# Optimization experiments

Hardware: AMD Instinct MI355X
Metric: run time of the kernel (lower is better)

The kernel has to match this reference:

```python
import jax, jax.numpy as jnp
import numpy as np

D_MODEL = 192; D_INNER = 384; D_STATE = 16; DT_RANK = 12; D_CONV = 4; DEPTH = 24
IMG = 256; PATCH = 16; BATCH = 32; NPATCH = (IMG // PATCH) ** 2; SEQ = NPATCH + 1; EPS = 1e-5


def setup_inputs() -> dict:
    key = jax.random.key(0)
    ks = iter(jax.random.split(key, 64))
    def rn(shape, s=0.02):
        return jax.random.normal(next(ks), shape, jnp.float32) * s
    inp = {}
    inp['x'] = jax.random.normal(next(ks), (BATCH, 3, IMG, IMG), jnp.float32)
    inp['patch_w'] = rn((D_MODEL, 3, PATCH, PATCH), 0.02)
    inp['patch_b'] = jnp.zeros((D_MODEL,), jnp.float32)
    inp['cls_token'] = rn((1, 1, D_MODEL), 0.02)
    inp['pos_embed'] = rn((1, SEQ, D_MODEL), 0.02)
    inp['norm_w'] = jnp.ones((DEPTH, D_MODEL), jnp.float32)
    inp['in_proj_w'] = rn((DEPTH, 2 * D_INNER, D_MODEL), 0.05)
    A_init = jnp.log(jnp.arange(1, D_STATE + 1, dtype=jnp.float32))  # S4D-real init
    for sfx in ['', '_b']:
        inp['conv_w' + sfx] = rn((DEPTH, D_INNER, D_CONV), 0.2)
        inp['conv_b' + sfx] = jnp.zeros((DEPTH, D_INNER), jnp.float32)
        inp['xproj_w' + sfx] = rn((DEPTH, DT_RANK + 2 * D_STATE, D_INNER), 0.05)
        inp['dtproj_w' + sfx] = rn((DEPTH, D_INNER, DT_RANK), 0.1)
        inp['dt_bias' + sfx] = rn((DEPTH, D_INNER), 0.5) - 4.0  # softplus(~-4) ~ small dt
        inp['A_log' + sfx] = jnp.broadcast_to(A_init, (DEPTH, D_INNER, D_STATE)).copy()
        inp['Dskip' + sfx] = jnp.ones((DEPTH, D_INNER), jnp.float32)
    inp['out_proj_w'] = rn((DEPTH, D_MODEL, D_INNER), 0.05)
    inp['norm_f_w'] = jnp.ones((D_MODEL,), jnp.float32)
    return inp


def _silu(v):
    return v * jax.nn.sigmoid(v)


def _rmsnorm(v, w):
    v = v.astype(jnp.float32)
    return v * jax.lax.rsqrt(jnp.mean(v * v, axis=-1, keepdims=True) + EPS) * w


def _ssm_branch(xin, z, conv_w, conv_b, xproj_w, dt_w, dt_b, A_log, Dp):
    # xin, z: (B, L, Di). One direction of the Mamba selective scan.
    B, L, Di = xin.shape
    pad = D_CONV - 1
    xp = jnp.pad(xin, ((0, 0), (pad, 0), (0, 0)))  # causal depthwise conv
    xc = sum(xp[:, k:k + L, :] * conv_w[:, k] for k in range(D_CONV)) + conv_b
    xc = _silu(xc)
    proj = jnp.einsum('bld,pd->blp', xc, xproj_w)  # (B,L,dt_rank+2N)
    dt_lo, Bm, Cm = jnp.split(proj, [DT_RANK, DT_RANK + D_STATE], axis=-1)
    dt = jax.nn.softplus(jnp.einsum('blr,dr->bld', dt_lo, dt_w) + dt_b)  # (B,L,Di)
    A = -jnp.exp(A_log)  # (Di, N)

    def step(h, inps):
        dt_t, B_t, C_t, x_t = inps  # (B,Di),(B,N),(B,N),(B,Di)
        dA = jnp.exp(dt_t[..., None] * A)                       # (B,Di,N)
        h = h * dA + (dt_t * x_t)[..., None] * B_t[:, None, :]  # ZOH discretization
        y = jnp.einsum('bdn,bn->bd', h, C_t)
        return h, y

    tm = lambda a: jnp.swapaxes(a, 0, 1)  # time-major
    h0 = jnp.zeros((B, Di, D_STATE), xin.dtype)
    _, ys = jax.lax.scan(step, h0, (tm(dt), tm(Bm), tm(Cm), tm(xc)))
    y = tm(ys) + Dp * xc
    return y * _silu(z)


def reference(x, patch_w, patch_b, cls_token, pos_embed, norm_w, in_proj_w,
              conv_w, conv_b, xproj_w, dtproj_w, dt_bias, A_log, Dskip,
              conv_w_b, conv_b_b, xproj_w_b, dtproj_w_b, dt_bias_b, A_log_b, Dskip_b,
              out_proj_w, norm_f_w):
    B = x.shape[0]
    # Patch embedding: Conv2d(3, D, k=16, s=16) -> (B, M, D)
    feat = jax.lax.conv_general_dilated(x, patch_w, (PATCH, PATCH), 'VALID',
                                        dimension_numbers=('NCHW', 'OIHW', 'NCHW'))
    feat = feat + patch_b[None, :, None, None]
    feat = feat.reshape(B, D_MODEL, NPATCH).transpose(0, 2, 1)
    # middle cls token insertion
    pos = NPATCH // 2
    cls = jnp.broadcast_to(cls_token, (B, 1, D_MODEL))
    h = jnp.concatenate([feat[:, :pos], cls, feat[:, pos:]], axis=1) + pos_embed
    residual = None
    flip = lambda a: a[:, ::-1]
    for i in range(DEPTH):
        # fused add + RMSNorm (prenorm), residual in fp32
        residual = h.astype(jnp.float32) if residual is None else (residual + h.astype(jnp.float32))
        hn = _rmsnorm(residual, norm_w[i])
        # Mamba mixer, bimamba v2 (shared in/out proj, separate scan params)
        xz = jnp.einsum('bld,ed->ble', hn, in_proj_w[i])
        xin, z = jnp.split(xz, 2, axis=-1)
        y_f = _ssm_branch(xin, z, conv_w[i], conv_b[i], xproj_w[i], dtproj_w[i],
                          dt_bias[i], A_log[i], Dskip[i])
        y_r = flip(_ssm_branch(flip(xin), flip(z), conv_w_b[i], conv_b_b[i], xproj_w_b[i],
                               dtproj_w_b[i], dt_bias_b[i], A_log_b[i], Dskip_b[i]))
        y = (y_f + y_r) * 0.5  # if_divide_out=True
        h = jnp.einsum('bld,od->blo', y, out_proj_w[i])
    # final fused add + RMSNorm (prenorm=False)
    out = _rmsnorm(residual + h.astype(jnp.float32), norm_f_w)
    return out
```

## Files before the change

### kernel.cpp

```cpp
#include <hip/hip_runtime.h>
#include <hip/hip_bf16.h>
#include <math.h>

#define D_MODEL 192
#define D_INNER 384
#define D_STATE 16
#define DT_RANK 12
#define DEPTH   24
#define SEQL    257
#define BATCH   32
#define NTOK    (BATCH*SEQL)
#define NC      16
#define CL      17
#define CCH     32

typedef unsigned short ushort_t;
using bf16x8 = __attribute__((ext_vector_type(8))) short;
using f32x4  = __attribute__((ext_vector_type(4))) float;

__device__ __forceinline__ ushort_t f2b(float f) {
    __hip_bfloat16 h = __float2bfloat16(f);
    return reinterpret_cast<ushort_t&>(h);
}
__device__ __forceinline__ float b2f(ushort_t u) {
    __hip_bfloat16 h;
    reinterpret_cast<ushort_t&>(h) = u;
    return __bfloat162float(h);
}
__device__ __forceinline__ float softplus_f(float v) {
    return (v > 20.f) ? v : log1pf(expf(v));
}
__device__ __forceinline__ float softplus_fast(float v) {
    float e = __expf(v);
    float lg = __logf(1.f + e);
    return (v > 20.f) ? v : lg;
}

__device__ __forceinline__ void pow_ladder(float r1, float* dA) {
    float r2 = r1 * r1;
    float r3 = r2 * r1;
    float r4 = r2 * r2;
    float r8 = r4 * r4;
    float r12 = r8 * r4;
    dA[0] = r1;       dA[1] = r2;       dA[2] = r3;       dA[3] = r4;
    dA[4] = r4 * r1;  dA[5] = r4 * r2;  dA[6] = r4 * r3;  dA[7] = r8;
    dA[8] = r8 * r1;  dA[9] = r8 * r2;  dA[10] = r8 * r3; dA[11] = r12;
    dA[12] = r12 * r1; dA[13] = r12 * r2; dA[14] = r12 * r3; dA[15] = r8 * r8;
}

__global__ __launch_bounds__(256) void convert_k(const float* __restrict__ in, ushort_t* __restrict__ out, int n) {
    int i = (blockIdx.x * 256 + threadIdx.x) * 4;
    if (i + 3 < n) {
        float4 v = *(const float4*)(in + i);
        ushort4 o;
        o.x = f2b(v.x); o.y = f2b(v.y); o.z = f2b(v.z); o.w = f2b(v.w);
        *(ushort4*)(out + i) = o;
    } else {
        for (int j = i; j < n; j++) out[j] = f2b(in[j]);
    }
}

__global__ __launch_bounds__(256) void checkA_k(const float* __restrict__ Al, const float* __restrict__ Alb,
                                                int* __restrict__ flag) {
    int i = blockIdx.x * 256 + threadIdx.x;
    const int total = DEPTH * 384 * 16;
    if (i >= total) return;
    int n = i & 15;
    float tgt = (float)(n + 1);
    float a = __expf(Al[i]);
    float b = __expf(Alb[i]);
    if (fabsf(a - tgt) > 1e-4f * tgt || fabsf(b - tgt) > 1e-4f * tgt) atomicAnd(flag, 0);
}

__global__ __launch_bounds__(256) void rearrange_k(const float* __restrict__ x, ushort_t* __restrict__ Ap) {
    size_t i = (size_t)blockIdx.x * 256 + threadIdx.x;
    const size_t total = (size_t)8192 * 768 / 4;
    if (i >= total) return;
    size_t o = i * 4;
    int bt  = (int)(o / 768);
    int rem = (int)(o % 768);
    int c  = rem >> 8;
    int r2 = rem & 255;
    int pi = r2 >> 4;
    int pj = r2 & 15;
    int b = bt >> 8;
    int t = bt & 255;
    int ph = t >> 4, pw = t & 15;
    size_t src = (((size_t)(b * 3 + c) * 256) + (size_t)(ph * 16 + pi)) * 256 + (pw * 16 + pj);
    float4 v = *(const float4*)(x + src);
    ushort4 ov;
    ov.x = f2b(v.x); ov.y = f2b(v.y); ov.z = f2b(v.z); ov.w = f2b(v.w);
    *(ushort4*)(Ap + o) = ov;
}

__global__ __launch_bounds__(192) void assemble_k(const float* __restrict__ P, const float* __restrict__ pb,
                                                  const float* __restrict__ cls, const float* __restrict__ pos,
                                                  float* __restrict__ hb) {
    int o = threadIdx.x;
    int l = blockIdx.x;
    int b = blockIdx.y;
    float v;
    if (l == 128) {
        v = cls[o];
    } else {
        int t = (l < 128) ? l : l - 1;
        v = P[((size_t)b * 256 + t) * 192 + o] + pb[o];
    }
    hb[((size_t)b * SEQL + l) * 192 + o] = v + pos[l * 192 + o];
}

template<int FINAL>
__global__ __launch_bounds__(192) void addnorm_k(float* res, const float* __restrict__ h,
                                                 const float* __restrict__ w, void* __restrict__ outp) {
    int row = blockIdx.x;
    int t = threadIdx.x;
    size_t idx = (size_t)row * 192 + t;
    float r = res[idx] + h[idx];
    if (!FINAL) res[idx] = r;
    float ss = r * r;
    #pragma unroll
    for (int o = 32; o > 0; o >>= 1) ss += __shfl_down(ss, o);
    __shared__ float ps[3];
    int wid = t >> 6;
    if ((t & 63) == 0) ps[wid] = ss;
    __syncthreads();
    float tot = ps[0] + ps[1] + ps[2];
    float inv = rsqrtf(tot / 192.f + 1e-5f);
    float v = r * inv * w[t];
    if (FINAL) ((float*)outp)[idx] = v;
    else       ((ushort_t*)outp)[idx] = f2b(v);
}

template<int OUTBF>
__global__ __launch_bounds__(256) void gemm_bf16(const ushort_t* __restrict__ A,
                                                 const ushort_t* __restrict__ W,
                                                 void* __restrict__ C,
                                                 int M, int N, int K, int ldc) {
    __shared__ ushort_t As[128 * 40];
    __shared__ ushort_t Bs[64 * 40];
    int tid = threadIdx.x;
    int m0 = blockIdx.y * 128, n0 = blockIdx.x * 64;
    int row = tid >> 2;
    int k8  = (tid & 3) * 8;
    int lane = tid & 63;
    int w = tid >> 6;
    int wr = w >> 1, wc = w & 1;
    int lr = lane & 15;
    int lk = (lane >> 4) * 8;
    f32x4 acc[4][2];
    #pragma unroll
    for (int i = 0; i < 4; i++)
        #pragma unroll
        for (int j = 0; j < 2; j++) acc[i][j] = (f32x4){0.f, 0.f, 0.f, 0.f};

    for (int k0 = 0; k0 < K; k0 += 32) {
        #pragma unroll
        for (int hhalf = 0; hhalf < 2; hhalf++) {
            int r = row + hhalf * 64;
            int m = m0 + r;
            bf16x8 v = {0,0,0,0,0,0,0,0};
            if (m < M) v = *(const bf16x8*)(A + (size_t)m * K + k0 + k8);
            *(bf16x8*)(&As[r * 40 + k8]) = v;
        }
        {
            int n = n0 + row;
            bf16x8 v = {0,0,0,0,0,0,0,0};
            if (n < N) v = *(const bf16x8*)(W + (size_t)n * K + k0 + k8);
            *(bf16x8*)(&Bs[row * 40 + k8]) = v;
        }
        __syncthreads();
        bf16x8 af[4], bfr[2];
        #pragma unroll
        for (int mi = 0; mi < 4; mi++)
            af[mi] = *(const bf16x8*)(&As[(wr * 64 + mi * 16 + lr) * 40 + lk]);
        #pragma unroll
        for (int ni = 0; ni < 2; ni++)
            bfr[ni] = *(const bf16x8*)(&Bs[(wc * 32 + ni * 16 + lr) * 40 + lk]);
        #pragma unroll
        for (int mi = 0; mi < 4; mi++)
            #pragma unroll
            for (int ni = 0; ni < 2; ni++)
                acc[mi][ni] = __builtin_amdgcn_mfma_f32_16x16x32_bf16(af[mi], bfr[ni], acc[mi][ni], 0, 0, 0);
        __syncthreads();
    }
    int rbase = (lane >> 4) * 4;
    #pragma unroll
    for (int mi = 0; mi < 4; mi++) {
        #pragma unroll
        for (int ni = 0; ni < 2; ni++) {
            #pragma unroll
            for (int r = 0; r < 4; r++) {
                int m = m0 + wr * 64 + mi * 16 + rbase + r;
                int n = n0 + wc * 32 + ni * 16 + lr;
                if (m < M && n < N) {
                    if (OUTBF) ((ushort_t*)C)[(size_t)m * ldc + n] = f2b(acc[mi][ni][r]);
                    else       ((float*)C)[(size_t)m * ldc + n] = acc[mi][ni][r];
                }
            }
        }
    }
}

__global__ __launch_bounds__(256) void gemm_xproj(const ushort_t* __restrict__ A0, const ushort_t* __restrict__ A1,
                                                  const ushort_t* __restrict__ W0, const ushort_t* __restrict__ W1,
                                                  float* __restrict__ C0, float* __restrict__ C1,
                                                  int M, int N, int K, int ldc) {
    __shared__ ushort_t As[64 * 40];
    __shared__ ushort_t Bs[64 * 40];
    int dir = blockIdx.z;
    const ushort_t* A = dir ? A1 : A0;
    const ushort_t* W = dir ? W1 : W0;
    float* C = dir ? C1 : C0;
    int tid = threadIdx.x;
    int m0 = blockIdx.y * 64, n0 = blockIdx.x * 64;
    int row = tid >> 2;
    int k8  = (tid & 3) * 8;
    int lane = tid & 63;
    int w = tid >> 6;
    int wr = w >> 1, wc = w & 1;
    int lr = lane & 15;
    int lk = (lane >> 4) * 8;
    f32x4 acc[2][2];
    #pragma unroll
    for (int i = 0; i < 2; i++)
        #pragma unroll
        for (int j = 0; j < 2; j++) acc[i][j] = (f32x4){0.f, 0.f, 0.f, 0.f};

    for (int k0 = 0; k0 < K; k0 += 32) {
        {
            int m = m0 + row;
            bf16x8 v = {0,0,0,0,0,0,0,0};
            if (m < M) v = *(const bf16x8*)(A + (size_t)m * K + k0 + k8);
            *(bf16x8*)(&As[row * 40 + k8]) = v;
            int n = n0 + row;
            bf16x8 wv = {0,0,0,0,0,0,0,0};
            if (n < N) wv = *(const bf16x8*)(W + (size_t)n * K + k0 + k8);
            *(bf16x8*)(&Bs[row * 40 + k8]) = wv;
        }
        __syncthreads();
        bf16x8 af[2], bfr[2];
        #pragma unroll
        for (int mi = 0; mi < 2; mi++)
            af[mi] = *(const bf16x8*)(&As[(wr * 32 + mi * 16 + lr) * 40 + lk]);
        #pragma unroll
        for (int ni = 0; ni < 2; ni++)
            bfr[ni] = *(const bf16x8*)(&Bs[(wc * 32 + ni * 16 + lr) * 40 + lk]);
        #pragma unroll
        for (int mi = 0; mi < 2; mi++)
            #pragma unroll
            for (int ni = 0; ni < 2; ni++)
                acc[mi][ni] = __builtin_amdgcn_mfma_f32_16x16x32_bf16(af[mi], bfr[ni], acc[mi][ni], 0, 0, 0);
        __syncthreads();
    }
    int rbase = (lane >> 4) * 4;
    #pragma unroll
    for (int mi = 0; mi < 2; mi++) {
        #pragma unroll
        for (int ni = 0; ni < 2; ni++) {
            #pragma unroll
            for (int r = 0; r < 4; r++) {
                int m = m0 + wr * 32 + mi * 16 + rbase + r;
                int n = n0 + wc * 32 + ni * 16 + lr;
                if (m < M && n < N) C[(size_t)m * ldc + n] = acc[mi][ni][r];
            }
        }
    }
}

__global__ __launch_bounds__(256) void gemm_out(const ushort_t* __restrict__ yf, const ushort_t* __restrict__ yr,
                                                const ushort_t* __restrict__ W, float* __restrict__ C,
                                                int M, int N, int K, int ldc) {
    __shared__ ushort_t As[64 * 40];
    __shared__ ushort_t Bs[64 * 40];
    int tid = threadIdx.x;
    int m0 = blockIdx.y * 64, n0 = blockIdx.x * 64;
    int row = tid >> 2;
    int k8  = (tid & 3) * 8;
    int lane = tid & 63;
    int w = tid >> 6;
    int wr = w >> 1, wc = w & 1;
    int lr = lane & 15;
    int lk = (lane >> 4) * 8;
    int m_ld = m0 + row;
    int mok = (m_ld < M);
    int bb = m_ld / SEQL;
    int ll = m_ld - bb * SEQL;
    size_t rowf = (size_t)m_ld * 384;
    size_t rowr = ((size_t)bb * SEQL + (SEQL - 1 - ll)) * 384;
    f32x4 acc[2][2];
    #pragma unroll
    for (int i = 0; i < 2; i++)
        #pragma unroll
        for (int j = 0; j < 2; j++) acc[i][j] = (f32x4){0.f, 0.f, 0.f, 0.f};

    for (int k0 = 0; k0 < K; k0 += 32) {
        {
            bf16x8 v = {0,0,0,0,0,0,0,0};
            if (mok) {
                bf16x8 vf = *(const bf16x8*)(yf + rowf + k0 + k8);
                bf16x8 vr = *(const bf16x8*)(yr + rowr + k0 + k8);
                #pragma unroll
                for (int j = 0; j < 8; j++) {
                    float a = b2f((ushort_t)vf[j]);
                    float b2 = b2f((ushort_t)vr[j]);
                    v[j] = (short)f2b(0.5f * (a + b2));
                }
            }
            *(bf16x8*)(&As[row * 40 + k8]) = v;
            int n = n0 + row;
            bf16x8 wv = {0,0,0,0,0,0,0,0};
            if (n < N) wv = *(const bf16x8*)(W + (size_t)n * K + k0 + k8);
            *(bf16x8*)(&Bs[row * 40 + k8]) = wv;
        }
        __syncthreads();
        bf16x8 af[2], bfr[2];
        #pragma unroll
        for (int mi = 0; mi < 2; mi++)
            af[mi] = *(const bf16x8*)(&As[(wr * 32 + mi * 16 + lr) * 40 + lk]);
        #pragma unroll
        for (int ni = 0; ni < 2; ni++)
            bfr[ni] = *(const bf16x8*)(&Bs[(wc * 32 + ni * 16 + lr) * 40 + lk]);
        #pragma unroll
        for (int mi = 0; mi < 2; mi++)
            #pragma unroll
            for (int ni = 0; ni < 2; ni++)
                acc[mi][ni] = __builtin_amdgcn_mfma_f32_16x16x32_bf16(af[mi], bfr[ni], acc[mi][ni], 0, 0, 0);
        __syncthreads();
    }
    int rbase = (lane >> 4) * 4;
    #pragma unroll
    for (int mi = 0; mi < 2; mi++) {
        #pragma unroll
        for (int ni = 0; ni < 2; ni++) {
            #pragma unroll
            for (int r = 0; r < 4; r++) {
                int m = m0 + wr * 32 + mi * 16 + rbase + r;
                int n = n0 + wc * 32 + ni * 16 + lr;
                if (m < M && n < N) C[(size_t)m * ldc + n] = acc[mi][ni][r];
            }
        }
    }
}

__global__ __launch_bounds__(384) void conv_silu_k(const ushort_t* __restrict__ xz,
                                                   const float* __restrict__ cw, const float* __restrict__ cb,
                                                   const float* __restrict__ cwb, const float* __restrict__ cbb,
                                                   ushort_t* __restrict__ xcf, ushort_t* __restrict__ xcr) {
    int d = threadIdx.x;
    int lc = blockIdx.x;
    int b = blockIdx.y;
    int dir = blockIdx.z;
    int lstart = lc * CCH;
    int lend = (lstart + CCH < SEQL) ? (lstart + CCH) : SEQL;
    const float* w = dir ? cwb : cw;
    const float* bias = dir ? cbb : cb;
    float4 wv = *(const float4*)(w + d * 4);
    float bs = bias[d];
    ushort_t* out = dir ? xcr : xcf;
    size_t base = (size_t)b * SEQL;
    float win0 = 0.f, win1 = 0.f, win2 = 0.f;
    if (lstart - 3 >= 0) win0 = b2f(xz[(base + (dir ? (SEQL-1-(lstart-3)) : (lstart-3))) * 768 + d]);
    if (lstart - 2 >= 0) win1 = b2f(xz[(base + (dir ? (SEQL-1-(lstart-2)) : (lstart-2))) * 768 + d]);
    if (lstart - 1 >= 0) win2 = b2f(xz[(base + (dir ? (SEQL-1-(lstart-1)) : (lstart-1))) * 768 + d]);
    float xcur = b2f(xz[(base + (dir ? (SEQL-1-lstart) : lstart)) * 768 + d]);
    for (int l = lstart; l < lend; l++) {
        int ln = l + 1;
        float xnext = 0.f;
        if (ln < lend) xnext = b2f(xz[(base + (dir ? (SEQL-1-ln) : ln)) * 768 + d]);
        float a = bs;
        a = fmaf(wv.x, win0, a);
        a = fmaf(wv.y, win1, a);
        a = fmaf(wv.z, win2, a);
        a = fmaf(wv.w, xcur, a);
        float s = a / (1.f + __expf(-a));
        out[(base + l) * 384 + d] = f2b(s);
        win0 = win1; win1 = win2; win2 = xcur; xcur = xnext;
    }
}

__global__ __launch_bounds__(192) void scan_p1(const ushort_t* __restrict__ xcf, const ushort_t* __restrict__ xcr,
                                               const float* __restrict__ dtbcf, const float* __restrict__ dtbcr,
                                               const float* __restrict__ dwf, const float* __restrict__ dwr,
                                               const float* __restrict__ dbf, const float* __restrict__ dbr,
                                               const float* __restrict__ Alf, const float* __restrict__ Alb,
                                               float* __restrict__ Sbuf, float* __restrict__ sumdt,
                                               const int* __restrict__ flagp) {
    int t = threadIdx.x;
    int d0 = t, d1 = t + 192;
    int c = blockIdx.x;
    int b = blockIdx.y, dir = blockIdx.z;
    int bd = b * 2 + dir;
    const ushort_t* xcp = dir ? xcr : xcf;
    const float* pbc = (dir ? dtbcr : dtbcf) + (size_t)b * SEQL * 44;
    int lstart = c * CL;
    int clen = (lstart + CL < SEQL) ? CL : (SEQL - lstart);
    size_t rowbase = (size_t)b * SEQL + lstart;

    float dw0[12], dw1[12];
    {
        const float* dwp = (dir ? dwr : dwf);
        #pragma unroll
        for (int r = 0; r < 12; r++) dw0[r] = dwp[d0 * 12 + r];
        #pragma unroll
        for (int r = 0; r < 12; r++) dw1[r] = dwp[d1 * 12 + r];
    }
    float db0 = (dir ? dbr : dbf)[d0];
    float db1 = (dir ? dbr : dbf)[d1];
    bool fast = (*flagp != 0);
    float S0[16], S1[16];
    #pragma unroll
    for (int n = 0; n < 16; n++) { S0[n] = 0.f; S1[n] = 0.f; }
    float ss0 = 0.f, ss1 = 0.f;

    if (fast) {
        float x0 = b2f(xcp[rowbase * 384 + d0]);
        float x1 = b2f(xcp[rowbase * 384 + d1]);
        for (int l = 0; l < clen; l++) {
            int ln = (l + 1 < clen) ? (l + 1) : l;
            float x0n = b2f(xcp[(rowbase + ln) * 384 + d0]);
            float x1n = b2f(xcp[(rowbase + ln) * 384 + d1]);
            const float* rp = pbc + (size_t)(lstart + l) * 44;
            float4 t0 = *(const float4*)(rp);
            float4 t1 = *(const float4*)(rp + 4);
            float4 t2 = *(const float4*)(rp + 8);
            float4 B0 = *(const float4*)(rp + 12);
            float4 B1 = *(const float4*)(rp + 16);
            float4 B2 = *(const float4*)(rp + 20);
            float4 B3 = *(const float4*)(rp + 24);
            float tv[12] = {t0.x,t0.y,t0.z,t0.w, t1.x,t1.y,t1.z,t1.w, t2.x,t2.y,t2.z,t2.w};
            float a0 = db0, a1 = db1;
            #pragma unroll
            for (int r = 0; r < 12; r++) {
                a0 = fmaf(tv[r], dw0[r], a0);
                a1 = fmaf(tv[r], dw1[r], a1);
            }
            float dt0 = softplus_fast(a0);
            float dt1 = softplus_fast(a1);
            ss0 += dt0; ss1 += dt1;
            float dtx0 = dt0 * x0, dtx1 = dt1 * x1;
            float dA0[16], dA1[16];
            pow_ladder(__expf(-dt0), dA0);
            pow_ladder(__expf(-dt1), dA1);
            float Bv[16] = {B0.x,B0.y,B0.z,B0.w, B1.x,B1.y,B1.z,B1.w,
                            B2.x,B2.y,B2.z,B2.w, B3.x,B3.y,B3.z,B3.w};
            #pragma unroll
            for (int n = 0; n < 16; n++) {
                S0[n] = fmaf(S0[n], dA0[n], dtx0 * Bv[n]);
                S1[n] = fmaf(S1[n], dA1[n], dtx1 * Bv[n]);
            }
            x0 = x0n; x1 = x1n;
        }
    } else {
        const float* alog = (dir ? Alb : Alf);
        float A0[16], A1[16];
        #pragma unroll
        for (int n = 0; n < 16; n++) A0[n] = -__expf(alog[d0 * 16 + n]);
        #pragma unroll
        for (int n = 0; n < 16; n++) A1[n] = -__expf(alog[d1 * 16 + n]);
        for (int l = 0; l < clen; l++) {
            const float* rp = pbc + (size_t)(lstart + l) * 44;
            float a0 = db0, a1 = db1;
            #pragma unroll
            for (int r = 0; r < 12; r++) {
                a0 = fmaf(rp[r], dw0[r], a0);
                a1 = fmaf(rp[r], dw1[r], a1);
            }
            float dt0 = softplus_f(a0);
            float dt1 = softplus_f(a1);
            ss0 += dt0; ss1 += dt1;
            float x0 = b2f(xcp[(rowbase + l) * 384 + d0]);
            float x1 = b2f(xcp[(rowbase + l) * 384 + d1]);
            float dtx0 = dt0 * x0, dtx1 = dt1 * x1;
            #pragma unroll
            for (int n = 0; n < 16; n++) {
                S0[n] = fmaf(S0[n], __expf(dt0 * A0[n]), dtx0 * rp[12 + n]);
                S1[n] = fmaf(S1[n], __expf(dt1 * A1[n]), dtx1 * rp[12 + n]);
            }
        }
    }
    float* spb = Sbuf + ((size_t)bd * NC + c) * 6144;
    #pragma unroll
    for (int j = 0; j < 4; j++) {
        *(float4*)(spb + d0 * 16 + j * 4) = make_float4(S0[j*4], S0[j*4+1], S0[j*4+2], S0[j*4+3]);
        *(float4*)(spb + d1 * 16 + j * 4) = make_float4(S1[j*4], S1[j*4+1], S1[j*4+2], S1[j*4+3]);
    }
    sumdt[((size_t)bd * NC + c) * 384 + d0] = ss0;
    sumdt[((size_t)bd * NC + c) * 384 + d1] = ss1;
}

__global__ __launch_bounds__(256) void scan_mid(float* __restrict__ Sbuf, const float* __restrict__ sumdt,
                                                const float* __restrict__ Alf, const float* __restrict__ Alb,
                                                const int* __restrict__ flagp) {
    int gid = blockIdx.x * 256 + threadIdx.x;
    int n = gid & 15;
    int rest = gid >> 4;
    int d = rest % 384;
    int bd = rest / 384;
    int dir = bd & 1;
    bool fast = (*flagp != 0);
    float A = fast ? -(float)(n + 1) : -__expf((dir ? Alb : Alf)[d * 16 + n]);
    float h = 0.f;
    #pragma unroll
    for (int c = 0; c < NC; c++) {
        size_t si = ((size_t)bd * NC + c) * 6144 + d * 16 + n;
        float S = Sbuf[si];
        float sd = sumdt[((size_t)bd * NC + c) * 384 + d];
        Sbuf[si] = h;
        h = fmaf(h, __expf(A * sd), S);
    }
}

__global__ __launch_bounds__(192) void scan_p3(const ushort_t* __restrict__ xcf, const ushort_t* __restrict__ xcr,
                                               const float* __restrict__ dtbcf, const float* __restrict__ dtbcr,
                                               const float* __restrict__ dwf, const float* __restrict__ dwr,
                                               const float* __restrict__ dbf, const float* __restrict__ dbr,
                                               const float* __restrict__ Alf, const float* __restrict__ Alb,
                                               const float* __restrict__ Df, const float* __restrict__ Db,
                                               const ushort_t* __restrict__ xz,
                                               const float* __restrict__ Sbuf,
                                               ushort_t* __restrict__ ybf, ushort_t* __restrict__ ybr,
                                               const int* __restrict__ flagp) {
    int t = threadIdx.x;
    int d0 = t, d1 = t + 192;
    int c = blockIdx.x;
    int b = blockIdx.y, dir = blockIdx.z;
    int bd = b * 2 + dir;
    const ushort_t* xcp = dir ? xcr : xcf;
    const float* pbc = (dir ? dtbcr : dtbcf) + (size_t)b * SEQL * 44;
    ushort_t* yb = dir ? ybr : ybf;
    int lstart = c * CL;
    int clen = (lstart + CL < SEQL) ? CL : (SEQL - lstart);
    size_t rowbase = (size_t)b * SEQL + lstart;
    size_t seqbase = (size_t)b * SEQL;

    float dw0[12], dw1[12];
    {
        const float* dwp = (dir ? dwr : dwf);
        #pragma unroll
        for (int r = 0; r < 12; r++) dw0[r] = dwp[d0 * 12 + r];
        #pragma unroll
        for (int r = 0; r < 12; r++) dw1[r] = dwp[d1 * 12 + r];
    }
    float db0 = (dir ? dbr : dbf)[d0];
    float db1 = (dir ? dbr : dbf)[d1];
    float Dp0 = (dir ? Db : Df)[d0];
    float Dp1 = (dir ? Db : Df)[d1];
    bool fast = (*flagp != 0);
    float h0[16], h1[16];
    {
        const float* spb = Sbuf + ((size_t)bd * NC + c) * 6144;
        #pragma unroll
        for (int j = 0; j < 4; j++) {
            float4 hv0 = *(const float4*)(spb + d0 * 16 + j * 4);
            float4 hv1 = *(const float4*)(spb + d1 * 16 + j * 4);
            h0[j*4] = hv0.x; h0[j*4+1] = hv0.y; h0[j*4+2] = hv0.z; h0[j*4+3] = hv0.w;
            h1[j*4] = hv1.x; h1[j*4+1] = hv1.y; h1[j*4+2] = hv1.z; h1[j*4+3] = hv1.w;
        }
    }

    if (fast) {
        float x0 = b2f(xcp[rowbase * 384 + d0]);
        float x1 = b2f(xcp[rowbase * 384 + d1]);
        size_t zr0 = (dir ? (seqbase + SEQL - 1 - lstart) : rowbase) * 768 + 384;
        float z0 = b2f(xz[zr0 + d0]);
        float z1 = b2f(xz[zr0 + d1]);
        for (int l = 0; l < clen; l++) {
            int ln = (l + 1 < clen) ? (l + 1) : l;
            float x0n = b2f(xcp[(rowbase + ln) * 384 + d0]);
            float x1n = b2f(xcp[(rowbase + ln) * 384 + d1]);
            size_t zrn = (dir ? (seqbase + SEQL - 1 - (lstart + ln)) : (rowbase + ln)) * 768 + 384;
            float z0n = b2f(xz[zrn + d0]);
            float z1n = b2f(xz[zrn + d1]);
            const float* rp = pbc + (size_t)(lstart + l) * 44;
            float4 t0 = *(const float4*)(rp);
            float4 t1 = *(const float4*)(rp + 4);
            float4 t2 = *(const float4*)(rp + 8);
            float4 B0 = *(const float4*)(rp + 12);
            float4 B1 = *(const float4*)(rp + 16);
            float4 B2 = *(const float4*)(rp + 20);
            float4 B3 = *(const float4*)(rp + 24);
            float4 C0 = *(const float4*)(rp + 28);
            float4 C1 = *(const float4*)(rp + 32);
            float4 C2 = *(const float4*)(rp + 36);
            float4 C3 = *(const float4*)(rp + 40);
            float tv[12] = {t0.x,t0.y,t0.z,t0.w, t1.x,t1.y,t1.z,t1.w, t2.x,t2.y,t2.z,t2.w};
            float a0 = db0, a1 = db1;
            #pragma unroll
            for (int r = 0; r < 12; r++) {
                a0 = fmaf(tv[r], dw0[r], a0);
                a1 = fmaf(tv[r], dw1[r], a1);
            }
            float dt0 = softplus_fast(a0);
            float dt1 = softplus_fast(a1);
            float dtx0 = dt0 * x0, dtx1 = dt1 * x1;
            float dA0[16], dA1[16];
            pow_ladder(__expf(-dt0), dA0);
            pow_ladder(__expf(-dt1), dA1);
            float Bv[16] = {B0.x,B0.y,B0.z,B0.w, B1.x,B1.y,B1.z,B1.w,
                            B2.x,B2.y,B2.z,B2.w, B3.x,B3.y,B3.z,B3.w};
            float Cv[16] = {C0.x,C0.y,C0.z,C0.w, C1.x,C1.y,C1.z,C1.w,
                            C2.x,C2.y,C2.z,C2.w, C3.x,C3.y,C3.z,C3.w};
            float y0 = 0.f, y1 = 0.f;
            #pragma unroll
            for (int n = 0; n < 16; n++) {
                h0[n] = fmaf(h0[n], dA0[n], dtx0 * Bv[n]);
                h1[n] = fmaf(h1[n], dA1[n], dtx1 * Bv[n]);
                y0 = fmaf(h0[n], Cv[n], y0);
                y1 = fmaf(h1[n], Cv[n], y1);
            }
            y0 = fmaf(Dp0, x0, y0);
            y1 = fmaf(Dp1, x1, y1);
            float sz0 = z0 / (1.f + __expf(-z0));
            float sz1 = z1 / (1.f + __expf(-z1));
            yb[(rowbase + l) * 384 + d0] = f2b(y0 * sz0);
            yb[(rowbase + l) * 384 + d1] = f2b(y1 * sz1);
            x0 = x0n; x1 = x1n; z0 = z0n; z1 = z1n;
        }
    } else {
        const float* alog = (dir ? Alb : Alf);
        float A0[16], A1[16];
        #pragma unroll
        for (int n = 0; n < 16; n++) A0[n] = -__expf(alog[d0 * 16 + n]);
        #pragma unroll
        for (int n = 0; n < 16; n++) A1[n] = -__expf(alog[d1 * 16 + n]);
        for (int l = 0; l < clen; l++) {
            const float* rp = pbc + (size_t)(lstart + l) * 44;
            float a0 = db0, a1 = db1;
            #pragma unroll
            for (int r = 0; r < 12; r++) {
                a0 = fmaf(rp[r], dw0[r], a0);
                a1 = fmaf(rp[r], dw1[r], a1);
            }
            float dt0 = softplus_f(a0);
            float dt1 = softplus_f(a1);
            float x0 = b2f(xcp[(rowbase + l) * 384 + d0]);
            float x1 = b2f(xcp[(rowbase + l) * 384 + d1]);
            size_t zr = (dir ? (seqbase + SEQL - 1 - (lstart + l)) : (rowbase + l)) * 768 + 384;
            float z0 = b2f(xz[zr + d0]);
            float z1 = b2f(xz[zr + d1]);
            float dtx0 = dt0 * x0, dtx1 = dt1 * x1;
            float y0 = 0.f, y1 = 0.f;
            #pragma unroll
            for (int n = 0; n < 16; n++) {
                h0[n] = fmaf(h0[n], __expf(dt0 * A0[n]), dtx0 * rp[12 + n]);
                h1[n] = fmaf(h1[n], __expf(dt1 * A1[n]), dtx1 * rp[12 + n]);
                y0 = fmaf(h0[n], rp[28 + n], y0);
                y1 = fmaf(h1[n], rp[28 + n], y1);
            }
            y0 = fmaf(Dp0, x0, y0);
            y1 = fmaf(Dp1, x1, y1);
            float sz0 = z0 / (1.f + __expf(-z0));
            float sz1 = z1 / (1.f + __expf(-z1));
            yb[(rowbase + l) * 384 + d0] = f2b(y0 * sz0);
            yb[(rowbase + l) * 384 + d1] = f2b(y1 * sz1);
        }
    }
}

extern "C" void kernel_launch(void* const* d_in, const int* in_sizes, int n_in,
                              void* d_out, int out_size, void* d_ws, size_t ws_size,
                              hipStream_t stream) {
    const float* x         = (const float*)d_in[0];
    const float* patch_w   = (const float*)d_in[1];
    const float* patch_b   = (const float*)d_in[2];
    const float* cls_token = (const float*)d_in[3];
    const float* pos_embed = (const float*)d_in[4];
    const float* norm_w    = (const float*)d_in[5];
    const float* in_proj_w = (const float*)d_in[6];
    const float* conv_w    = (const float*)d_in[7];
    const float* conv_b    = (const float*)d_in[8];
    const float* xproj_w   = (const float*)d_in[9];
    const float* dtproj_w  = (const float*)d_in[10];
    const float* dt_bias   = (const float*)d_in[11];
    const float* A_log     = (const float*)d_in[12];
    const float* Dskip     = (const float*)d_in[13];
    const float* conv_w_b  = (const float*)d_in[14];
    const float* conv_b_b  = (const float*)d_in[15];
    const float* xproj_w_b = (const float*)d_in[16];
    const float* dtproj_w_b= (const float*)d_in[17];
    const float* dt_bias_b = (const float*)d_in[18];
    const float* A_log_b   = (const float*)d_in[19];
    const float* Dskip_b   = (const float*)d_in[20];
    const float* out_proj_w= (const float*)d_in[21];
    const float* norm_f_w  = (const float*)d_in[22];

    float* ws = (float*)d_ws;
    size_t off = 0;
    float* res   = ws + off; off += (size_t)NTOK * 192;
    float* hbuf  = ws + off; off += (size_t)NTOK * 192;
    ushort_t* xzb = (ushort_t*)(ws + off); off += (size_t)NTOK * 384;
    ushort_t* hnb = (ushort_t*)(ws + off); off += (size_t)NTOK * 96;
    ushort_t* xcfb = (ushort_t*)(ws + off); off += (size_t)NTOK * 192;
    ushort_t* xcrb = (ushort_t*)(ws + off); off += (size_t)NTOK * 192;
    float* dtbcf = ws + off; off += (size_t)NTOK * 44;
    float* dtbcr = ws + off; off += (size_t)NTOK * 44;
    ushort_t* ybf = (ushort_t*)(ws + off); off += (size_t)NTOK * 192;
    ushort_t* ybr = (ushort_t*)(ws + off); off += (size_t)NTOK * 192;
    float* Sbuf  = ws + off; off += (size_t)BATCH * 2 * NC * 6144;
    float* sumdt = ws + off; off += (size_t)BATCH * 2 * NC * 384;
    int* flagp   = (int*)(ws + off); off += 4;
    ushort_t* wb = (ushort_t*)(ws + off);
    ushort_t* winb   = wb;
    ushort_t* woutb  = winb  + 3538944;
    ushort_t* xpfb   = woutb + 1769472;
    ushort_t* xprb   = xpfb  + 405504;
    ushort_t* patchwb= xprb  + 405504;

    ushort_t* Apatch = xzb;
    float* Ppatch = Sbuf;

    convert_k<<<(3538944/4 + 255)/256, 256, 0, stream>>>(in_proj_w, winb, 3538944);
    convert_k<<<(1769472/4 + 255)/256, 256, 0, stream>>>(out_proj_w, woutb, 1769472);
    convert_k<<<(405504/4 + 255)/256, 256, 0, stream>>>(xproj_w, xpfb, 405504);
    convert_k<<<(405504/4 + 255)/256, 256, 0, stream>>>(xproj_w_b, xprb, 405504);
    convert_k<<<(147456/4 + 255)/256, 256, 0, stream>>>(patch_w, patchwb, 147456);

    hipMemsetAsync(res, 0, (size_t)NTOK * 192 * sizeof(float), stream);
    hipMemsetAsync(flagp, 1, 4, stream);
    checkA_k<<<(DEPTH*384*16 + 255)/256, 256, 0, stream>>>(A_log, A_log_b, flagp);

    rearrange_k<<<6144, 256, 0, stream>>>(x, Apatch);
    gemm_bf16<0><<<dim3(3, 64), 256, 0, stream>>>(Apatch, patchwb, Ppatch, 8192, 192, 768, 192);
    assemble_k<<<dim3(SEQL, BATCH), 192, 0, stream>>>(Ppatch, patch_b, cls_token, pos_embed, hbuf);

    for (int i = 0; i < DEPTH; i++) {
        const float* nw   = norm_w + i * 192;
        const float* cwf  = conv_w + (size_t)i * 384 * 4;
        const float* cbf  = conv_b + (size_t)i * 384;
        const float* cwr  = conv_w_b + (size_t)i * 384 * 4;
        const float* cbr  = conv_b_b + (size_t)i * 384;
        const float* dpf  = dtproj_w + (size_t)i * 384 * 12;
        const float* dpr  = dtproj_w_b + (size_t)i * 384 * 12;
        const float* dbf  = dt_bias + (size_t)i * 384;
        const float* dbr  = dt_bias_b + (size_t)i * 384;
        const float* alf  = A_log + (size_t)i * 384 * 16;
        const float* alr  = A_log_b + (size_t)i * 384 * 16;
        const float* dsf  = Dskip + (size_t)i * 384;
        const float* dsr  = Dskip_b + (size_t)i * 384;

        addnorm_k<0><<<NTOK, 192, 0, stream>>>(res, hbuf, nw, hnb);
        gemm_bf16<1><<<dim3(12, 65), 256, 0, stream>>>(hnb, winb + (size_t)i * 768 * 192, xzb,
                                                       NTOK, 768, 192, 768);
        conv_silu_k<<<dim3((SEQL + CCH - 1) / CCH, BATCH, 2), 384, 0, stream>>>(xzb, cwf, cbf, cwr, cbr, xcfb, xcrb);
        gemm_xproj<<<dim3(1, 129, 2), 256, 0, stream>>>(xcfb, xcrb,
                                                        xpfb + (size_t)i * 44 * 384, xprb + (size_t)i * 44 * 384,
                                                        dtbcf, dtbcr, NTOK, 44, 384, 44);
        scan_p1<<<dim3(NC, BATCH, 2), 192, 0, stream>>>(xcfb, xcrb, dtbcf, dtbcr,
                                                        dpf, dpr, dbf, dbr, alf, alr, Sbuf, sumdt, flagp);
        scan_mid<<<(BATCH * 2 * 384 * 16) / 256, 256, 0, stream>>>(Sbuf, sumdt, alf, alr, flagp);
        scan_p3<<<dim3(NC, BATCH, 2), 192, 0, stream>>>(xcfb, xcrb, dtbcf, dtbcr,
                                                        dpf, dpr, dbf, dbr, alf, alr, dsf, dsr,
                                                        xzb, Sbuf, ybf, ybr, flagp);
        gemm_out<<<dim3(3, 129), 256, 0, stream>>>(ybf, ybr, woutb + (size_t)i * 192 * 384, hbuf,
                                                   NTOK, 192, 384, 192);
    }

    addnorm_k<1><<<NTOK, 192, 0, stream>>>(res, hbuf, norm_f_w, (float*)d_out);
}
```

Measured before the change: 3.051 ms.

## Fuse out-projection GEMM with residual add and next-layer RMSNorm

Replaces the separate out_proj GEMM and the following add+RMSNorm kernel with one kernel whose blocks each cover 32 full rows of all 192 output columns. The residual add and row norm are done in the GEMM epilogue through shuffle and shared-memory reductions. This removes one launch per layer and the round trip of the fp32 hbuf through memory. In exchange the GEMM tile shape changes to 32x192, and only half the threads load A, which may lower load efficiency. NTOK/32 divides evenly, so no bounds checks are needed.

```diff
diff --git a/kernel.cpp b/kernel.cpp
--- a/kernel.cpp
+++ b/kernel.cpp
@@ -109,14 +109,13 @@
     hb[((size_t)b * SEQL + l) * 192 + o] = v + pos[l * 192 + o];
 }
 
-template<int FINAL>
 __global__ __launch_bounds__(192) void addnorm_k(float* res, const float* __restrict__ h,
-                                                 const float* __restrict__ w, void* __restrict__ outp) {
+                                                 const float* __restrict__ w, ushort_t* __restrict__ outp) {
     int row = blockIdx.x;
     int t = threadIdx.x;
     size_t idx = (size_t)row * 192 + t;
     float r = res[idx] + h[idx];
-    if (!FINAL) res[idx] = r;
+    res[idx] = r;
     float ss = r * r;
     #pragma unroll
     for (int o = 32; o > 0; o >>= 1) ss += __shfl_down(ss, o);
@@ -126,9 +125,7 @@
     __syncthreads();
     float tot = ps[0] + ps[1] + ps[2];
     float inv = rsqrtf(tot / 192.f + 1e-5f);
-    float v = r * inv * w[t];
-    if (FINAL) ((float*)outp)[idx] = v;
-    else       ((ushort_t*)outp)[idx] = f2b(v);
+    outp[idx] = f2b(r * inv * w[t]);
 }
 
 template<int OUTBF>
@@ -267,76 +264,132 @@
     }
 }
 
-__global__ __launch_bounds__(256) void gemm_out(const ushort_t* __restrict__ yf, const ushort_t* __restrict__ yr,
-                                                const ushort_t* __restrict__ W, float* __restrict__ C,
-                                                int M, int N, int K, int ldc) {
-    __shared__ ushort_t As[64 * 40];
-    __shared__ ushort_t Bs[64 * 40];
+template<int FINAL>
+__global__ __launch_bounds__(256) void gemm_outnorm(const ushort_t* __restrict__ yf, const ushort_t* __restrict__ yr,
+                                                    const ushort_t* __restrict__ W, float* __restrict__ res,
+                                                    const float* __restrict__ nw, void* __restrict__ outp) {
+    __shared__ ushort_t As[32 * 40];
+    __shared__ ushort_t Bs[192 * 40];
+    __shared__ float psums[4 * 32];
+    const int K = 384;
     int tid = threadIdx.x;
-    int m0 = blockIdx.y * 64, n0 = blockIdx.x * 64;
-    int row = tid >> 2;
-    int k8  = (tid & 3) * 8;
+    int m0 = blockIdx.y * 32;
     int lane = tid & 63;
     int w = tid >> 6;
-    int wr = w >> 1, wc = w & 1;
     int lr = lane & 15;
-    int lk = (lane >> 4) * 8;
-    int m_ld = m0 + row;
-    int mok = (m_ld < M);
-    int bb = m_ld / SEQL;
-    int ll = m_ld - bb * SEQL;
-    size_t rowf = (size_t)m_ld * 384;
-    size_t rowr = ((size_t)bb * SEQL + (SEQL - 1 - ll)) * 384;
-    f32x4 acc[2][2];
+    int hi2 = lane >> 4;
+    int lk = hi2 * 8;
+    f32x4 acc[2][3];
     #pragma unroll
     for (int i = 0; i < 2; i++)
         #pragma unroll
-        for (int j = 0; j < 2; j++) acc[i][j] = (f32x4){0.f, 0.f, 0.f, 0.f};
+        for (int j = 0; j < 3; j++) acc[i][j] = (f32x4){0.f, 0.f, 0.f, 0.f};
+
+    int arow = tid >> 2;
+    int k8 = (tid & 3) * 8;
+    size_t rowfA = 0, rowrA = 0;
+    if (tid < 128) {
+        int m_ld = m0 + arow;
+        int bb = m_ld / SEQL;
+        int ll = m_ld - bb * SEQL;
+        rowfA = (size_t)m_ld * 384;
+        rowrA = ((size_t)bb * SEQL + (SEQL - 1 - ll)) * 384;
+    }
 
     for (int k0 = 0; k0 < K; k0 += 32) {
-        {
-            bf16x8 v = {0,0,0,0,0,0,0,0};
-            if (mok) {
-                bf16x8 vf = *(const bf16x8*)(yf + rowf + k0 + k8);
-                bf16x8 vr = *(const bf16x8*)(yr + rowr + k0 + k8);
-                #pragma unroll
-                for (int j = 0; j < 8; j++) {
-                    float a = b2f((ushort_t)vf[j]);
-                    float b2 = b2f((ushort_t)vr[j]);
-                    v[j] = (short)f2b(0.5f * (a + b2));
-                }
-            }
-            *(bf16x8*)(&As[row * 40 + k8]) = v;
-            int n = n0 + row;
-            bf16x8 wv = {0,0,0,0,0,0,0,0};
-            if (n < N) wv = *(const bf16x8*)(W + (size_t)n * K + k0 + k8);
-            *(bf16x8*)(&Bs[row * 40 + k8]) = wv;
+        if (tid < 128) {
+            bf16x8 vf = *(const bf16x8*)(yf + rowfA + k0 + k8);
+            bf16x8 vr = *(const bf16x8*)(yr + rowrA + k0 + k8);
+            bf16x8 v;
+            #pragma unroll
+            for (int j = 0; j < 8; j++) {
+                float a = b2f((ushort_t)vf[j]);
+                float b2 = b2f((ushort_t)vr[j]);
+                v[j] = (short)f2b(0.5f * (a + b2));
+            }
+            *(bf16x8*)(&As[arow * 40 + k8]) = v;
+        }
+        #pragma unroll
+        for (int s = 0; s < 3; s++) {
+            int n = arow + s * 64;
+            *(bf16x8*)(&Bs[n * 40 + k8]) = *(const bf16x8*)(W + (size_t)n * K + k0 + k8);
         }
         __syncthreads();
-        bf16x8 af[2], bfr[2];
+        bf16x8 af[2], bfr[3];
         #pragma unroll
         for (int mi = 0; mi < 2; mi++)
-            af[mi] = *(const bf16x8*)(&As[(wr * 32 + mi * 16 + lr) * 40 + lk]);
-        #pragma unroll
-        for (int ni = 0; ni < 2; ni++)
-            bfr[ni] = *(const bf16x8*)(&Bs[(wc * 32 + ni * 16 + lr) * 40 + lk]);
+            af[mi] = *(const bf16x8*)(&As[(mi * 16 + lr) * 40 + lk]);
+        #pragma unroll
+        for (int ni = 0; ni < 3; ni++)
+            bfr[ni] = *(const bf16x8*)(&Bs[(w * 48 + ni * 16 + lr) * 40 + lk]);
         #pragma unroll
         for (int mi = 0; mi < 2; mi++)
             #pragma unroll
-            for (int ni = 0; ni < 2; ni++)
+            for (int ni = 0; ni < 3; ni++)
                 acc[mi][ni] = __builtin_amdgcn_mfma_f32_16x16x32_bf16(af[mi], bfr[ni], acc[mi][ni], 0, 0, 0);
         __syncthreads();
     }
-    int rbase = (lane >> 4) * 4;
+
     #pragma unroll
     for (int mi = 0; mi < 2; mi++) {
         #pragma unroll
-        for (int ni = 0; ni < 2; ni++) {
+        for (int r = 0; r < 4; r++) {
+            int m = m0 + mi * 16 + hi2 * 4 + r;
+            #pragma unroll
+            for (int ni = 0; ni < 3; ni++) {
+                int col = w * 48 + ni * 16 + lr;
+                acc[mi][ni][r] += res[(size_t)m * 192 + col];
+            }
+        }
+    }
+    float pp[2][4];
+    #pragma unroll
+    for (int mi = 0; mi < 2; mi++)
+        #pragma unroll
+        for (int r = 0; r < 4; r++) {
+            float s = acc[mi][0][r] * acc[mi][0][r];
+            s = fmaf(acc[mi][1][r], acc[mi][1][r], s);
+            s = fmaf(acc[mi][2][r], acc[mi][2][r], s);
+            pp[mi][r] = s;
+        }
+    #pragma unroll
+    for (int mask = 1; mask < 16; mask <<= 1)
+        #pragma unroll
+        for (int mi = 0; mi < 2; mi++)
+            #pragma unroll
+            for (int r = 0; r < 4; r++)
+                pp[mi][r] += __shfl_xor(pp[mi][r], mask);
+    if (lr == 0) {
+        #pragma unroll
+        for (int mi = 0; mi < 2; mi++)
+            #pragma unroll
+            for (int r = 0; r < 4; r++)
+                psums[w * 32 + mi * 16 + hi2 * 4 + r] = pp[mi][r];
+    }
+    __syncthreads();
+    float inv[2][4];
+    #pragma unroll
+    for (int mi = 0; mi < 2; mi++)
+        #pragma unroll
+        for (int r = 0; r < 4; r++) {
+            int idx = mi * 16 + hi2 * 4 + r;
+            float tot = psums[idx] + psums[32 + idx] + psums[64 + idx] + psums[96 + idx];
+            inv[mi][r] = rsqrtf(tot / 192.f + 1e-5f);
+        }
+    #pragma unroll
+    for (int mi = 0; mi < 2; mi++) {
+        #pragma unroll
+        for (int ni = 0; ni < 3; ni++) {
+            int col = w * 48 + ni * 16 + lr;
+            float nwc = nw[col];
             #pragma unroll
             for (int r = 0; r < 4; r++) {
-                int m = m0 + wr * 32 + mi * 16 + rbase + r;
-                int n = n0 + wc * 32 + ni * 16 + lr;
-                if (m < M && n < N) C[(size_t)m * ldc + n] = acc[mi][ni][r];
+                int m = m0 + mi * 16 + hi2 * 4 + r;
+                float v = acc[mi][ni][r];
+                if (!FINAL) res[(size_t)m * 192 + col] = v;
+                float o = v * inv[mi][r] * nwc;
+                if (FINAL) ((float*)outp)[(size_t)m * 192 + col] = o;
+                else       ((ushort_t*)outp)[(size_t)m * 192 + col] = f2b(o);
             }
         }
     }
@@ -722,9 +775,9 @@
     rearrange_k<<<6144, 256, 0, stream>>>(x, Apatch);
     gemm_bf16<0><<<dim3(3, 64), 256, 0, stream>>>(Apatch, patchwb, Ppatch, 8192, 192, 768, 192);
     assemble_k<<<dim3(SEQL, BATCH), 192, 0, stream>>>(Ppatch, patch_b, cls_token, pos_embed, hbuf);
+    addnorm_k<<<NTOK, 192, 0, stream>>>(res, hbuf, norm_w, hnb);
 
     for (int i = 0; i < DEPTH; i++) {
-        const float* nw   = norm_w + i * 192;
         const float* cwf  = conv_w + (size_t)i * 384 * 4;
         const float* cbf  = conv_b + (size_t)i * 384;
         const float* cwr  = conv_w_b + (size_t)i * 384 * 4;
@@ -738,7 +791,6 @@
         const float* dsf  = Dskip + (size_t)i * 384;
         const float* dsr  = Dskip_b + (size_t)i * 384;
 
-        addnorm_k<0><<<NTOK, 192, 0, stream>>>(res, hbuf, nw, hnb);
         gemm_bf16<1><<<dim3(12, 65), 256, 0, stream>>>(hnb, winb + (size_t)i * 768 * 192, xzb,
                                                        NTOK, 768, 192, 768);
         conv_silu_k<<<dim3((SEQL + CCH - 1) / CCH, BATCH, 2), 384, 0, stream>>>(xzb, cwf, cbf, cwr, cbr, xcfb, xcrb);
@@ -751,9 +803,12 @@
         scan_p3<<<dim3(NC, BATCH, 2), 192, 0, stream>>>(xcfb, xcrb, dtbcf, dtbcr,
                                                         dpf, dpr, dbf, dbr, alf, alr, dsf, dsr,
                                                         xzb, Sbuf, ybf, ybr, flagp);
-        gemm_out<<<dim3(3, 129), 256, 0, stream>>>(ybf, ybr, woutb + (size_t)i * 192 * 384, hbuf,
-                                                   NTOK, 192, 384, 192);
-    }
-
-    addnorm_k<1><<<NTOK, 192, 0, stream>>>(res, hbuf, norm_f_w, (float*)d_out);
-}
+        if (i < DEPTH - 1) {
+            gemm_outnorm<0><<<dim3(1, NTOK / 32), 256, 0, stream>>>(ybf, ybr, woutb + (size_t)i * 192 * 384,
+                                                                    res, norm_w + (size_t)(i + 1) * 192, hnb);
+        } else {
+            gemm_outnorm<1><<<dim3(1, NTOK / 32), 256, 0, stream>>>(ybf, ybr, woutb + (size_t)i * 192 * 384,
+                                                                    res, norm_f_w, (float*)d_out);
+        }
+    }
+}
```

New measurement: 2.989 ms, median of 2. 2.0% less time.
